# Performance work log

Measured on AMD Instinct MI355X. Metric: run time of the kernel, lower is better.

Reference implementation:

```python
import jax, jax.numpy as jnp
import numpy as np

B, C, H, W = 4, 256, 64, 64
C8 = C // 8


def setup_inputs() -> dict:
    key = jax.random.key(0)
    ks = jax.random.split(key, 8)
    x = jax.random.normal(ks[0], (B, C, H, W), dtype=jnp.float32)
    # 1x1 conv weights act as per-pixel linear maps: [out_ch, in_ch]
    Wq = jax.random.normal(ks[1], (C8, C), dtype=jnp.float32) * 0.05
    bq = jax.random.normal(ks[2], (C8,), dtype=jnp.float32) * 0.01
    Wk = jax.random.normal(ks[3], (C8, C), dtype=jnp.float32) * 0.05
    bk = jax.random.normal(ks[4], (C8,), dtype=jnp.float32) * 0.01
    Wv = jax.random.normal(ks[5], (C, C), dtype=jnp.float32) * 0.05
    bv = jax.random.normal(ks[6], (C,), dtype=jnp.float32) * 0.01
    # torch inits gamma to 0 (identity); use nonzero so output exercises the attention path
    gamma = jnp.array(0.5, dtype=jnp.float32)
    return {"x": x, "Wq": Wq, "bq": bq, "Wk": Wk, "bk": bk, "Wv": Wv, "bv": bv, "gamma": gamma}


def reference(x, Wq, bq, Wk, bk, Wv, bv, gamma):
    b, c, h, w = x.shape
    n = h * w
    xf = x.reshape(b, c, n)                                   # [B,C,N]
    q = jnp.einsum('oc,bcn->bno', Wq, xf) + bq                # [B,N,C8] (proj_query permuted)
    k = jnp.einsum('oc,bcn->bon', Wk, xf) + bk[:, None]       # [B,C8,N]
    energy = jnp.einsum('bnc,bcm->bnm', q, k)                 # [B,N_q,N_k]
    # NOTE: torch Softmax(dim=1) -> normalize over the QUERY axis (axis=1)
    attention = jax.nn.softmax(energy, axis=1)
    v = jnp.einsum('oc,bcn->bon', Wv, xf) + bv[:, None]       # [B,C,N]
    out = jnp.einsum('bcn,bnm->bcm', v, attention).reshape(b, c, h, w)
    return gamma * out + x
```

## Files before the change

kernel.cpp:

```cpp
#include <hip/hip_runtime.h>
#include <hip/hip_bf16.h>

#define BN 4
#define CC 256
#define C8 32
#define NN 4096
#define PROJ_ROWS 320

typedef __attribute__((ext_vector_type(8))) short short8;
typedef __attribute__((ext_vector_type(4))) float f32x4;
typedef __attribute__((ext_vector_type(4))) unsigned short u16x4;

__device__ __forceinline__ unsigned short f2bf(float f) {
    unsigned u = __builtin_bit_cast(unsigned, f);
    unsigned r = (u + 0x7fffu + ((u >> 16) & 1u)) >> 16;
    return (unsigned short)r;
}

__device__ __forceinline__ float bf2f(unsigned short s) {
    return __builtin_bit_cast(float, ((unsigned)s) << 16);
}

__global__ __launch_bounds__(256) void proj_kernel(
    const float* __restrict__ x,
    const float* __restrict__ Wq, const float* __restrict__ bq,
    const float* __restrict__ Wk, const float* __restrict__ bk,
    const float* __restrict__ Wv, const float* __restrict__ bv,
    unsigned short* __restrict__ proj, unsigned short* __restrict__ qT)
{
    int bid = blockIdx.x;
    int b = bid >> 6, nt = bid & 63;
    int n0 = nt * 64;
    int tid = threadIdx.x;
    int w = tid >> 6, l = tid & 63, l15 = l & 15, lq = l >> 4;

    __shared__ alignas(16) unsigned short Xt[64][264];

    int c_l = tid >> 3;
    int nb  = (tid & 7) * 8;

#pragma unroll
    for (int kc = 0; kc < 8; kc++) {
        const float* xp = x + ((size_t)(b * CC + kc * 32 + c_l)) * NN + n0 + nb;
        float4 x0 = *(const float4*)xp;
        float4 x1 = *(const float4*)(xp + 4);
        float t[8] = {x0.x, x0.y, x0.z, x0.w, x1.x, x1.y, x1.z, x1.w};
#pragma unroll
        for (int e = 0; e < 8; e++) Xt[nb + e][kc * 32 + c_l] = f2bf(t[e]);
    }
    __syncthreads();

    f32x4 acc[5][4];
#pragma unroll
    for (int gi = 0; gi < 5; gi++)
#pragma unroll
        for (int mi = 0; mi < 4; mi++) acc[gi][mi] = (f32x4){0.f, 0.f, 0.f, 0.f};

    for (int kc = 0; kc < 8; kc++) {
        float4 wf[5][2];
#pragma unroll
        for (int gi = 0; gi < 5; gi++) {
            int og = (w * 5 + gi) * 16 + l15;
            const float* wrow = (og < 32) ? (Wq + (size_t)og * CC)
                              : (og < 64) ? (Wk + (size_t)(og - 32) * CC)
                                          : (Wv + (size_t)(og - 64) * CC);
            const float* wp = wrow + kc * 32 + lq * 8;
            wf[gi][0] = *(const float4*)wp;
            wf[gi][1] = *(const float4*)(wp + 4);
        }
#pragma unroll
        for (int gi = 0; gi < 5; gi++) {
            unsigned short a8[8] __attribute__((aligned(16)));
            float tw[8] = {wf[gi][0].x, wf[gi][0].y, wf[gi][0].z, wf[gi][0].w,
                           wf[gi][1].x, wf[gi][1].y, wf[gi][1].z, wf[gi][1].w};
#pragma unroll
            for (int e = 0; e < 8; e++) a8[e] = f2bf(tw[e]);
            short8 af = *(const short8*)a8;
#pragma unroll
            for (int mi = 0; mi < 4; mi++) {
                short8 bf = *(const short8*)&Xt[mi * 16 + l15][kc * 32 + lq * 8];
                acc[gi][mi] = __builtin_amdgcn_mfma_f32_16x16x32_bf16(af, bf, acc[gi][mi], 0, 0, 0);
            }
        }
    }

#pragma unroll
    for (int gi = 0; gi < 5; gi++) {
#pragma unroll
        for (int r = 0; r < 4; r++) {
            int og = (w * 5 + gi) * 16 + lq * 4 + r;
            float bias = (og < 32) ? bq[og] : (og < 64) ? bk[og - 32] : bv[og - 64];
#pragma unroll
            for (int mi = 0; mi < 4; mi++) {
                int n = n0 + mi * 16 + l15;
                unsigned short v16 = f2bf(acc[gi][mi][r] + bias);
                if (og < 32) {
                    qT[((size_t)b * NN + n) * C8 + og] = v16;
                } else {
                    proj[((size_t)b * PROJ_ROWS + og) * NN + n] = v16;
                }
            }
        }
    }
}

template<int NSPLIT, bool FINAL>
__global__ __launch_bounds__(256, 4) void attn_kernel(
    const unsigned short* __restrict__ proj,
    const unsigned short* __restrict__ qT,
    const float* __restrict__ x,
    const float* __restrict__ gamma_p,
    float* __restrict__ out,
    unsigned short* __restrict__ Opart,
    float* __restrict__ Lpart)
{
    constexpr int ITERS = 64 / NSPLIT;
    int bid = blockIdx.x;
    int h   = bid >> 8;
    int low = bid & 255;
    int xcd = low & 7;
    int b = xcd >> 1;
    int mtile = ((low >> 3) << 1) | (xcd & 1);
    int m0 = mtile * 64;
    int nbase = h * (ITERS * 64);

    int tid = threadIdx.x;
    int w = tid >> 6, l = tid & 63, l15 = l & 15, lq = l >> 4;

    __shared__ alignas(16) unsigned short ps[2][64][72];
    __shared__ float red[4][64];
    __shared__ float Ltot[64];

    const unsigned short* kbase = proj + ((size_t)b * PROJ_ROWS + C8) * NN;
    const unsigned short* vbase = proj + ((size_t)b * PROJ_ROWS + 64) * NN;
    const unsigned short* qbase = qT + (size_t)b * NN * C8;

    short8 kfrag[4];
#pragma unroll
    for (int mi = 0; mi < 4; mi++) {
        int col = m0 + mi * 16 + l15;
        unsigned short t8[8] __attribute__((aligned(16)));
#pragma unroll
        for (int j = 0; j < 8; j++)
            t8[j] = kbase[(size_t)(lq * 8 + j) * NN + col];
        kfrag[mi] = *(const short8*)t8;
    }

    f32x4 O[4][4];
#pragma unroll
    for (int ci = 0; ci < 4; ci++)
#pragma unroll
        for (int mi = 0; mi < 4; mi++) O[ci][mi] = (f32x4){0.f, 0.f, 0.f, 0.f};
    float runS[4] = {0.f, 0.f, 0.f, 0.f};

    {
        short8 qfrag = *(const short8*)(qbase + (size_t)(nbase + 16 * w + l15) * C8 + lq * 8);
#pragma unroll
        for (int mi = 0; mi < 4; mi++) {
            f32x4 S = __builtin_amdgcn_mfma_f32_16x16x32_bf16(
                qfrag, kfrag[mi], (f32x4){0.f, 0.f, 0.f, 0.f}, 0, 0, 0);
            float p0 = __expf(S[0]);
            float p1 = __expf(S[1]);
            float p2 = __expf(S[2]);
            float p3 = __expf(S[3]);
            runS[mi] += (p0 + p1) + (p2 + p3);
            unsigned pk0 = (unsigned)f2bf(p0) | ((unsigned)f2bf(p1) << 16);
            unsigned pk1 = (unsigned)f2bf(p2) | ((unsigned)f2bf(p3) << 16);
            *(uint2*)&ps[0][mi * 16 + l15][16 * w + lq * 4] = make_uint2(pk0, pk1);
        }
    }

    for (int it = 0; it < ITERS; it++) {
        int n0c = nbase + it * 64;
        __syncthreads();

        const unsigned short* psrc = &ps[it & 1][0][0];
#pragma unroll
        for (int kh = 0; kh < 2; kh++) {
            short8 av[4];
#pragma unroll
            for (int ci = 0; ci < 4; ci++)
                av[ci] = *(const short8*)(vbase
                         + (size_t)(64 * w + ci * 16 + l15) * NN + n0c + kh * 32 + lq * 8);
            short8 bfr[4];
#pragma unroll
            for (int mi = 0; mi < 4; mi++)
                bfr[mi] = *(const short8*)(psrc + (mi * 16 + l15) * 72 + kh * 32 + lq * 8);
#pragma unroll
            for (int ci = 0; ci < 4; ci++)
#pragma unroll
                for (int mi = 0; mi < 4; mi++)
                    O[ci][mi] = __builtin_amdgcn_mfma_f32_16x16x32_bf16(
                        av[ci], bfr[mi], O[ci][mi], 0, 0, 0);
        }

        if (it + 1 < ITERS) {
            short8 qfrag = *(const short8*)(qbase
                           + (size_t)(n0c + 64 + 16 * w + l15) * C8 + lq * 8);
            unsigned short* pdst = &ps[(it + 1) & 1][0][0];
#pragma unroll
            for (int mi = 0; mi < 4; mi++) {
                f32x4 S = __builtin_amdgcn_mfma_f32_16x16x32_bf16(
                    qfrag, kfrag[mi], (f32x4){0.f, 0.f, 0.f, 0.f}, 0, 0, 0);
                float p0 = __expf(S[0]);
                float p1 = __expf(S[1]);
                float p2 = __expf(S[2]);
                float p3 = __expf(S[3]);
                runS[mi] += (p0 + p1) + (p2 + p3);
                unsigned pk0 = (unsigned)f2bf(p0) | ((unsigned)f2bf(p1) << 16);
                unsigned pk1 = (unsigned)f2bf(p2) | ((unsigned)f2bf(p3) << 16);
                *(uint2*)(pdst + (mi * 16 + l15) * 72 + 16 * w + lq * 4) = make_uint2(pk0, pk1);
            }
        }
    }

#pragma unroll
    for (int mi = 0; mi < 4; mi++) {
        float s = runS[mi];
        s += __shfl_xor(s, 16);
        s += __shfl_xor(s, 32);
        red[w][mi * 16 + l15] = s;
    }
    __syncthreads();
    if (tid < 64) Ltot[tid] = red[0][tid] + red[1][tid] + red[2][tid] + red[3][tid];
    __syncthreads();

    if constexpr (FINAL) {
        float gamma = gamma_p[0];
        float iv[4];
#pragma unroll
        for (int mi = 0; mi < 4; mi++) iv[mi] = 1.0f / Ltot[mi * 16 + l15];
#pragma unroll
        for (int ci = 0; ci < 4; ci++) {
#pragma unroll
            for (int mi = 0; mi < 4; mi++) {
                int m = m0 + mi * 16 + l15;
#pragma unroll
                for (int r = 0; r < 4; r++) {
                    int c = 64 * w + ci * 16 + lq * 4 + r;
                    size_t idx = ((size_t)b * CC + c) * NN + m;
                    out[idx] = gamma * (O[ci][mi][r] * iv[mi]) + x[idx];
                }
            }
        }
    } else {
        size_t p = ((size_t)h * BN + b) * 64 + mtile;
        if (tid < 64) Lpart[p * 64 + tid] = Ltot[tid];
        unsigned short* Ob = Opart + p * (size_t)(CC * 64);
#pragma unroll
        for (int ci = 0; ci < 4; ci++) {
#pragma unroll
            for (int mi = 0; mi < 4; mi++) {
#pragma unroll
                for (int r = 0; r < 4; r++) {
                    int c = 64 * w + ci * 16 + lq * 4 + r;
                    Ob[c * 64 + mi * 16 + l15] = f2bf(O[ci][mi][r]);
                }
            }
        }
    }
}

template<int NSPLIT>
__global__ __launch_bounds__(256) void combine_kernel(
    const unsigned short* __restrict__ Opart, const float* __restrict__ Lpart,
    const float* __restrict__ x, const float* __restrict__ gamma_p,
    float* __restrict__ out)
{
    int bid = blockIdx.x;
    int cq = bid & 3;
    int mt = (bid >> 2) & 63;
    int b  = bid >> 8;
    int tid = threadIdx.x;
    int m4 = tid & 15, c16 = tid >> 4;
    float gamma = gamma_p[0];

    f32x4 Ls = (f32x4){0.f, 0.f, 0.f, 0.f};
#pragma unroll
    for (int h = 0; h < NSPLIT; h++) {
        size_t p = ((size_t)h * BN + b) * 64 + mt;
        Ls += *(const f32x4*)(Lpart + p * 64 + m4 * 4);
    }
    f32x4 inv;
#pragma unroll
    for (int j = 0; j < 4; j++) inv[j] = 1.0f / Ls[j];

#pragma unroll
    for (int cp = 0; cp < 4; cp++) {
        int c = cq * 64 + cp * 16 + c16;
        f32x4 acc = (f32x4){0.f, 0.f, 0.f, 0.f};
#pragma unroll
        for (int h = 0; h < NSPLIT; h++) {
            size_t p = ((size_t)h * BN + b) * 64 + mt;
            u16x4 o4 = *(const u16x4*)(Opart + p * (size_t)(CC * 64) + c * 64 + m4 * 4);
#pragma unroll
            for (int j = 0; j < 4; j++) acc[j] += bf2f(o4[j]);
        }
        size_t idx = ((size_t)b * CC + c) * NN + mt * 64 + m4 * 4;
        f32x4 xv = *(const f32x4*)(x + idx);
        f32x4 o;
#pragma unroll
        for (int j = 0; j < 4; j++) o[j] = gamma * (acc[j] * inv[j]) + xv[j];
        *(f32x4*)(out + idx) = o;
    }
}

extern "C" void kernel_launch(void* const* d_in, const int* in_sizes, int n_in,
                              void* d_out, int out_size, void* d_ws, size_t ws_size,
                              hipStream_t stream) {
    const float* x     = (const float*)d_in[0];
    const float* Wq    = (const float*)d_in[1];
    const float* bq    = (const float*)d_in[2];
    const float* Wk    = (const float*)d_in[3];
    const float* bk    = (const float*)d_in[4];
    const float* Wv    = (const float*)d_in[5];
    const float* bv    = (const float*)d_in[6];
    const float* gamma = (const float*)d_in[7];
    float* out = (float*)d_out;
    (void)in_sizes; (void)n_in; (void)out_size;

    unsigned short* proj = (unsigned short*)d_ws;
    unsigned short* qT   = proj + (size_t)BN * PROJ_ROWS * NN;
    const size_t baseB = ((size_t)BN * PROJ_ROWS * NN + (size_t)BN * NN * C8) * 2;

    auto needB = [&](int ns) {
        size_t LpB = (size_t)ns * BN * 64 * 64 * 4;
        size_t OpB = (size_t)ns * BN * 64 * CC * 64 * 2;
        return baseB + LpB + OpB;
    };

    proj_kernel<<<256, 256, 0, stream>>>(x, Wq, bq, Wk, bk, Wv, bv, proj, qT);

    if (ws_size >= needB(4)) {
        float* Lpart = (float*)((char*)d_ws + baseB);
        unsigned short* Opart = (unsigned short*)(Lpart + (size_t)4 * BN * 64 * 64);
        attn_kernel<4, false><<<1024, 256, 0, stream>>>(proj, qT, x, gamma, out, Opart, Lpart);
        combine_kernel<4><<<1024, 256, 0, stream>>>(Opart, Lpart, x, gamma, out);
    } else if (ws_size >= needB(2)) {
        float* Lpart = (float*)((char*)d_ws + baseB);
        unsigned short* Opart = (unsigned short*)(Lpart + (size_t)2 * BN * 64 * 64);
        attn_kernel<2, false><<<512, 256, 0, stream>>>(proj, qT, x, gamma, out, Opart, Lpart);
        combine_kernel<2><<<1024, 256, 0, stream>>>(Opart, Lpart, x, gamma, out);
    } else {
        attn_kernel<1, true><<<256, 256, 0, stream>>>(proj, qT, x, gamma, out, nullptr, nullptr);
    }
}
```

Baseline: 175.9 us.

## Compute P fragments per wave in registers, removing shared memory and barriers

Each wave now computes the full 64-query exp tile for its own key columns directly in registers. The packed bf16 P values feed the PV MFMA as B-fragments, which removes the shared-memory ping-pong buffer, the per-iteration __syncthreads, and the cross-wave reduction of the softmax denominator. V loads are split into two 4-element halves to match the fragment layout, and bf16 packing uses the hardware v_cvt_pk_bf16_f32 instruction. The trade-off is that QK^T and exp work is duplicated across all four waves, and the launch-bounds occupancy hint is lowered from 4 to 3 to allow more registers.

Result: slower. 265.7 us (+51.1%).

```diff
diff --git a/kernel.cpp b/kernel.cpp
--- a/kernel.cpp
+++ b/kernel.cpp
@@ -10,6 +10,7 @@
 typedef __attribute__((ext_vector_type(8))) short short8;
 typedef __attribute__((ext_vector_type(4))) float f32x4;
 typedef __attribute__((ext_vector_type(4))) unsigned short u16x4;
+typedef __attribute__((ext_vector_type(4))) unsigned int u32x4;
 
 __device__ __forceinline__ unsigned short f2bf(float f) {
     unsigned u = __builtin_bit_cast(unsigned, f);
@@ -19,6 +20,12 @@
 
 __device__ __forceinline__ float bf2f(unsigned short s) {
     return __builtin_bit_cast(float, ((unsigned)s) << 16);
+}
+
+__device__ __forceinline__ unsigned cvtpk(float lo, float hi) {
+    unsigned r;
+    asm("v_cvt_pk_bf16_f32 %0, %1, %2" : "=v"(r) : "v"(lo), "v"(hi));
+    return r;
 }
 
 __global__ __launch_bounds__(256) void proj_kernel(
@@ -105,7 +112,7 @@
 }
 
 template<int NSPLIT, bool FINAL>
-__global__ __launch_bounds__(256, 4) void attn_kernel(
+__global__ __launch_bounds__(256, 3) void attn_kernel(
     const unsigned short* __restrict__ proj,
     const unsigned short* __restrict__ qT,
     const float* __restrict__ x,
@@ -127,13 +134,9 @@
     int tid = threadIdx.x;
     int w = tid >> 6, l = tid & 63, l15 = l & 15, lq = l >> 4;
 
-    __shared__ alignas(16) unsigned short ps[2][64][72];
-    __shared__ float red[4][64];
-    __shared__ float Ltot[64];
-
     const unsigned short* kbase = proj + ((size_t)b * PROJ_ROWS + C8) * NN;
     const unsigned short* vbase = proj + ((size_t)b * PROJ_ROWS + 64) * NN;
-    const unsigned short* qbase = qT + (size_t)b * NN * C8;
+    const unsigned short* qlane = qT + (size_t)b * NN * C8 + (size_t)l15 * C8 + lq * 8;
 
     short8 kfrag[4];
 #pragma unroll
@@ -146,6 +149,11 @@
         kfrag[mi] = *(const short8*)t8;
     }
 
+    const unsigned short* vrow[4];
+#pragma unroll
+    for (int ci = 0; ci < 4; ci++)
+        vrow[ci] = vbase + (size_t)(64 * w + ci * 16 + l15) * NN;
+
     f32x4 O[4][4];
 #pragma unroll
     for (int ci = 0; ci < 4; ci++)
@@ -153,83 +161,94 @@
         for (int mi = 0; mi < 4; mi++) O[ci][mi] = (f32x4){0.f, 0.f, 0.f, 0.f};
     float runS[4] = {0.f, 0.f, 0.f, 0.f};
 
-    {
-        short8 qfrag = *(const short8*)(qbase + (size_t)(nbase + 16 * w + l15) * C8 + lq * 8);
-#pragma unroll
-        for (int mi = 0; mi < 4; mi++) {
-            f32x4 S = __builtin_amdgcn_mfma_f32_16x16x32_bf16(
-                qfrag, kfrag[mi], (f32x4){0.f, 0.f, 0.f, 0.f}, 0, 0, 0);
-            float p0 = __expf(S[0]);
-            float p1 = __expf(S[1]);
-            float p2 = __expf(S[2]);
-            float p3 = __expf(S[3]);
-            runS[mi] += (p0 + p1) + (p2 + p3);
-            unsigned pk0 = (unsigned)f2bf(p0) | ((unsigned)f2bf(p1) << 16);
-            unsigned pk1 = (unsigned)f2bf(p2) | ((unsigned)f2bf(p3) << 16);
-            *(uint2*)&ps[0][mi * 16 + l15][16 * w + lq * 4] = make_uint2(pk0, pk1);
-        }
-    }
-
     for (int it = 0; it < ITERS; it++) {
         int n0c = nbase + it * 64;
-        __syncthreads();
-
-        const unsigned short* psrc = &ps[it & 1][0][0];
-#pragma unroll
-        for (int kh = 0; kh < 2; kh++) {
-            short8 av[4];
-#pragma unroll
-            for (int ci = 0; ci < 4; ci++)
-                av[ci] = *(const short8*)(vbase
-                         + (size_t)(64 * w + ci * 16 + l15) * NN + n0c + kh * 32 + lq * 8);
-            short8 bfr[4];
+
+        short8 qf0 = *(const short8*)(qlane + (size_t)(n0c)      * C8);
+        short8 qf1 = *(const short8*)(qlane + (size_t)(n0c + 16) * C8);
+        short8 qf2 = *(const short8*)(qlane + (size_t)(n0c + 32) * C8);
+        short8 qf3 = *(const short8*)(qlane + (size_t)(n0c + 48) * C8);
+
+        uint2 avlo[4], avhi[4];
+#pragma unroll
+        for (int ci = 0; ci < 4; ci++) {
+            avlo[ci] = *(const uint2*)(vrow[ci] + n0c + 4 * lq);
+            avhi[ci] = *(const uint2*)(vrow[ci] + n0c + 16 + 4 * lq);
+        }
+
+        short8 bfrA[4];
+#pragma unroll
+        for (int mi = 0; mi < 4; mi++) {
+            f32x4 S0 = __builtin_amdgcn_mfma_f32_16x16x32_bf16(
+                qf0, kfrag[mi], (f32x4){0.f, 0.f, 0.f, 0.f}, 0, 0, 0);
+            f32x4 S1 = __builtin_amdgcn_mfma_f32_16x16x32_bf16(
+                qf1, kfrag[mi], (f32x4){0.f, 0.f, 0.f, 0.f}, 0, 0, 0);
+            float p0 = __expf(S0[0]), p1 = __expf(S0[1]);
+            float p2 = __expf(S0[2]), p3 = __expf(S0[3]);
+            float p4 = __expf(S1[0]), p5 = __expf(S1[1]);
+            float p6 = __expf(S1[2]), p7 = __expf(S1[3]);
+            runS[mi] += ((p0 + p1) + (p2 + p3)) + ((p4 + p5) + (p6 + p7));
+            u32x4 pk = (u32x4){cvtpk(p0, p1), cvtpk(p2, p3),
+                               cvtpk(p4, p5), cvtpk(p6, p7)};
+            bfrA[mi] = __builtin_bit_cast(short8, pk);
+        }
+#pragma unroll
+        for (int ci = 0; ci < 4; ci++) {
+            short8 av = __builtin_bit_cast(short8,
+                (u32x4){avlo[ci].x, avlo[ci].y, avhi[ci].x, avhi[ci].y});
 #pragma unroll
             for (int mi = 0; mi < 4; mi++)
-                bfr[mi] = *(const short8*)(psrc + (mi * 16 + l15) * 72 + kh * 32 + lq * 8);
-#pragma unroll
-            for (int ci = 0; ci < 4; ci++)
-#pragma unroll
-                for (int mi = 0; mi < 4; mi++)
-                    O[ci][mi] = __builtin_amdgcn_mfma_f32_16x16x32_bf16(
-                        av[ci], bfr[mi], O[ci][mi], 0, 0, 0);
-        }
-
-        if (it + 1 < ITERS) {
-            short8 qfrag = *(const short8*)(qbase
-                           + (size_t)(n0c + 64 + 16 * w + l15) * C8 + lq * 8);
-            unsigned short* pdst = &ps[(it + 1) & 1][0][0];
-#pragma unroll
-            for (int mi = 0; mi < 4; mi++) {
-                f32x4 S = __builtin_amdgcn_mfma_f32_16x16x32_bf16(
-                    qfrag, kfrag[mi], (f32x4){0.f, 0.f, 0.f, 0.f}, 0, 0, 0);
-                float p0 = __expf(S[0]);
-                float p1 = __expf(S[1]);
-                float p2 = __expf(S[2]);
-                float p3 = __expf(S[3]);
-                runS[mi] += (p0 + p1) + (p2 + p3);
-                unsigned pk0 = (unsigned)f2bf(p0) | ((unsigned)f2bf(p1) << 16);
-                unsigned pk1 = (unsigned)f2bf(p2) | ((unsigned)f2bf(p3) << 16);
-                *(uint2*)(pdst + (mi * 16 + l15) * 72 + 16 * w + lq * 4) = make_uint2(pk0, pk1);
-            }
-        }
-    }
-
+                O[ci][mi] = __builtin_amdgcn_mfma_f32_16x16x32_bf16(
+                    av, bfrA[mi], O[ci][mi], 0, 0, 0);
+        }
+
+#pragma unroll
+        for (int ci = 0; ci < 4; ci++) {
+            avlo[ci] = *(const uint2*)(vrow[ci] + n0c + 32 + 4 * lq);
+            avhi[ci] = *(const uint2*)(vrow[ci] + n0c + 48 + 4 * lq);
+        }
+
+        short8 bfrB[4];
+#pragma unroll
+        for (int mi = 0; mi < 4; mi++) {
+            f32x4 S2 = __builtin_amdgcn_mfma_f32_16x16x32_bf16(
+                qf2, kfrag[mi], (f32x4){0.f, 0.f, 0.f, 0.f}, 0, 0, 0);
+            f32x4 S3 = __builtin_amdgcn_mfma_f32_16x16x32_bf16(
+                qf3, kfrag[mi], (f32x4){0.f, 0.f, 0.f, 0.f}, 0, 0, 0);
+            float p0 = __expf(S2[0]), p1 = __expf(S2[1]);
+            float p2 = __expf(S2[2]), p3 = __expf(S2[3]);
+            float p4 = __expf(S3[0]), p5 = __expf(S3[1]);
+            float p6 = __expf(S3[2]), p7 = __expf(S3[3]);
+            runS[mi] += ((p0 + p1) + (p2 + p3)) + ((p4 + p5) + (p6 + p7));
+            u32x4 pk = (u32x4){cvtpk(p0, p1), cvtpk(p2, p3),
+                               cvtpk(p4, p5), cvtpk(p6, p7)};
+            bfrB[mi] = __builtin_bit_cast(short8, pk);
+        }
+#pragma unroll
+        for (int ci = 0; ci < 4; ci++) {
+            short8 av = __builtin_bit_cast(short8,
+                (u32x4){avlo[ci].x, avlo[ci].y, avhi[ci].x, avhi[ci].y});
+#pragma unroll
+            for (int mi = 0; mi < 4; mi++)
+                O[ci][mi] = __builtin_amdgcn_mfma_f32_16x16x32_bf16(
+                    av, bfrB[mi], O[ci][mi], 0, 0, 0);
+        }
+    }
+
+    float rs[4];
 #pragma unroll
     for (int mi = 0; mi < 4; mi++) {
-        float s = runS[mi];
-        s += __shfl_xor(s, 16);
-        s += __shfl_xor(s, 32);
-        red[w][mi * 16 + l15] = s;
-    }
-    __syncthreads();
-    if (tid < 64) Ltot[tid] = red[0][tid] + red[1][tid] + red[2][tid] + red[3][tid];
-    __syncthreads();
+        float s2 = runS[mi];
+        s2 += __shfl_xor(s2, 16);
+        s2 += __shfl_xor(s2, 32);
+        rs[mi] = s2;
+    }
 
     if constexpr (FINAL) {
         float gamma = gamma_p[0];
         float iv[4];
 #pragma unroll
-        for (int mi = 0; mi < 4; mi++) iv[mi] = 1.0f / Ltot[mi * 16 + l15];
+        for (int mi = 0; mi < 4; mi++) iv[mi] = 1.0f / rs[mi];
 #pragma unroll
         for (int ci = 0; ci < 4; ci++) {
 #pragma unroll
@@ -245,7 +264,11 @@
         }
     } else {
         size_t p = ((size_t)h * BN + b) * 64 + mtile;
-        if (tid < 64) Lpart[p * 64 + tid] = Ltot[tid];
+        if (w == 0 && lq == 0) {
+#pragma unroll
+            for (int mi = 0; mi < 4; mi++)
+                Lpart[p * 64 + mi * 16 + l15] = rs[mi];
+        }
         unsigned short* Ob = Opart + p * (size_t)(CC * 64);
 #pragma unroll
         for (int ci = 0; ci < 4; ci++) {
```
